# Optimization experiments

Hardware: AMD Instinct MI355X
Metric: run time of the kernel (lower is better)

Reference implementation:

```python
import jax, jax.numpy as jnp
import numpy as np

L, B, F, E, H, V, NL, K = 32, 128, 4096, 512, 512, 50000, 2, 20


def setup_inputs() -> dict:
    key = jax.random.key(0)
    ks = jax.random.split(key, 9)
    return {
        "dialog_encoder_inputs": jax.random.randint(ks[0], (L, B), 0, V),
        "fact_inputs": jax.random.normal(ks[1], (B, F, E), dtype=jnp.float32),
        "h": jax.random.normal(ks[2], (NL, B, H), dtype=jnp.float32),
        "c": jax.random.normal(ks[3], (NL, B, H), dtype=jnp.float32),
        "enc_emb": jax.random.normal(ks[4], (V, E), dtype=jnp.float32) * 0.02,
        "Aw": jax.random.normal(ks[5], (H, E), dtype=jnp.float32) * 0.04,
        "Ab": jnp.zeros((H,), dtype=jnp.float32),
        "Cw": jax.random.normal(ks[6], (H, E), dtype=jnp.float32) * 0.04,
        "Cb": jnp.zeros((H,), dtype=jnp.float32),
        "top_k": K,
    }


def reference(dialog_encoder_inputs, fact_inputs, h, c, enc_emb, Aw, Ab, Cw, Cb, top_k):
    # --- get_top_k_fact_average: embed dialog, score facts, gather top-k ---
    q = enc_emb[dialog_encoder_inputs].mean(axis=0)                # [B, E] mean-pooled query
    scores = jnp.einsum('be,bfe->bf', q, fact_inputs)              # [B, F] similarity
    _, idx = jax.lax.top_k(scores, top_k)                          # [B, K]
    topf = jnp.take_along_axis(fact_inputs, idx[:, :, None], axis=1)  # [B, K, E]

    # --- facts_forward: memory-network style hidden-state update ---
    fact_M = jnp.einsum('bke,he->bkh', topf, Aw) + Ab              # fact_linearA
    fact_C = jnp.einsum('bke,he->bkh', topf, Cw) + Cb              # fact_linearC

    def update(u):  # u: [NL, B, H]
        P = jax.nn.softmax(jnp.einsum('bke,lbe->lbk', topf, u), axis=-1)  # attn over facts
        o = jnp.einsum('lbk,bke->lbe', P, topf)                           # weighted fact avg
        return o + u

    return update(h), update(c), fact_M, fact_C
```

## Files before the change

kernel.cpp:

```cpp
#include <hip/hip_runtime.h>
#include <float.h>
#include <math.h>

#define LL 32
#define BB 128
#define FF 4096
#define EE 512
#define HH 512
#define NLAYER 2
#define KK 20

typedef float f4 __attribute__((ext_vector_type(4)));
typedef short bf16x8 __attribute__((ext_vector_type(8)));
typedef float f32x4 __attribute__((ext_vector_type(4)));

__device__ inline unsigned short bf16rne(float x) {
    unsigned u = __float_as_uint(x);
    u += 0x7fff + ((u >> 16) & 1);
    return (unsigned short)(u >> 16);
}

__global__ __launch_bounds__(256) void prep_kernel(const int* __restrict__ tok,
                                                   const float* __restrict__ emb,
                                                   float* __restrict__ q,
                                                   const float* __restrict__ Aw,
                                                   const float* __restrict__ Cw,
                                                   unsigned short* __restrict__ Wbf) {
    int bid = blockIdx.x;
    if (bid < 256) {
        int b = bid >> 1, eh = bid & 1;
        __shared__ int ts[LL];
        if (threadIdx.x < LL) ts[threadIdx.x] = tok[threadIdx.x * BB + b];
        __syncthreads();
        int e = eh * 256 + threadIdx.x;
        float acc = 0.f;
        #pragma unroll
        for (int l = 0; l < LL; ++l) acc += emb[(long)ts[l] * EE + e];
        q[b * EE + e] = acc * (1.0f / LL);
    } else {
        int cid = bid - 256;
        int matY = cid >> 8;
        int blkX = cid & 255;
        const float* W = matY ? Cw : Aw;
        unsigned short* dst = Wbf + (size_t)matY * HH * EE;
        int i = (blkX * 256 + threadIdx.x) * 4;
        float4 v = *(const float4*)(W + i);
        ushort4 o;
        o.x = bf16rne(v.x); o.y = bf16rne(v.y); o.z = bf16rne(v.z); o.w = bf16rne(v.w);
        *(ushort4*)(dst + i) = o;
    }
}

__global__ __launch_bounds__(256) void scores_kernel(const float* __restrict__ q,
                                                     const float* __restrict__ fact,
                                                     float* __restrict__ scores) {
    int b = blockIdx.y;
    int wave = threadIdx.x >> 6;
    int lane = threadIdx.x & 63;
    const f4* qv = (const f4*)(q + b * EE);
    f4 qa = qv[lane];
    f4 qb = qv[64 + lane];
    int f0 = (blockIdx.x * 4 + wave) * 8;
    float d[8];
    #pragma unroll
    for (int i = 0; i < 8; ++i) {
        const f4* fv = (const f4*)(fact + ((long)b * FF + f0 + i) * EE);
        f4 fa = __builtin_nontemporal_load(fv + lane);
        f4 fb = __builtin_nontemporal_load(fv + 64 + lane);
        f4 p = qa * fa + qb * fb;
        d[i] = p.x + p.y + p.z + p.w;
    }
    bool h32 = lane & 32;
    float e0, e1, e2, e3;
    {
        float s0 = __shfl_xor(d[0], 32), s1 = __shfl_xor(d[1], 32);
        float s2 = __shfl_xor(d[2], 32), s3 = __shfl_xor(d[3], 32);
        float s4 = __shfl_xor(d[4], 32), s5 = __shfl_xor(d[5], 32);
        float s6 = __shfl_xor(d[6], 32), s7 = __shfl_xor(d[7], 32);
        e0 = h32 ? d[4] + s4 : d[0] + s0;
        e1 = h32 ? d[5] + s5 : d[1] + s1;
        e2 = h32 ? d[6] + s6 : d[2] + s2;
        e3 = h32 ? d[7] + s7 : d[3] + s3;
    }
    bool h16 = lane & 16;
    float g0, g1;
    {
        float s0 = __shfl_xor(e0, 16), s1 = __shfl_xor(e1, 16);
        float s2 = __shfl_xor(e2, 16), s3 = __shfl_xor(e3, 16);
        g0 = h16 ? e2 + s2 : e0 + s0;
        g1 = h16 ? e3 + s3 : e1 + s1;
    }
    bool h8 = lane & 8;
    float hs;
    {
        float s0 = __shfl_xor(g0, 8), s1 = __shfl_xor(g1, 8);
        hs = h8 ? g1 + s1 : g0 + s0;
    }
    hs += __shfl_xor(hs, 4);
    hs += __shfl_xor(hs, 2);
    hs += __shfl_xor(hs, 1);
    if ((lane & 7) == 0) scores[b * FF + f0 + ((lane >> 3) & 7)] = hs;
}

__global__ __launch_bounds__(256) void fused_kernel(const float* __restrict__ scores,
                                                    const float* __restrict__ fact,
                                                    const float* __restrict__ hin,
                                                    const float* __restrict__ cin,
                                                    const unsigned short* __restrict__ Wbf,
                                                    const float* __restrict__ Ab,
                                                    const float* __restrict__ Cb,
                                                    float* __restrict__ out) {
    int b = blockIdx.x;
    __shared__ float vals[FF];
    __shared__ float tf[KK][EE];
    __shared__ unsigned short tfb[32 * EE];
    __shared__ unsigned long long wbest[4];
    __shared__ int sel[KK];
    int t = threadIdx.x;
    int wave = t >> 6, lane = t & 63;

    const float4* sv = (const float4*)(scores + b * FF);
    float4* vv = (float4*)vals;
    for (int i = t; i < FF / 4; i += 256) vv[i] = sv[i];
    {
        float4 z = {0, 0, 0, 0};
        for (int i = t; i < 12 * 1024 / 16; i += 256)
            *(float4*)((char*)tfb + 20 * 1024 + i * 16) = z;
    }
    __syncthreads();

    for (int it = 0; it < KK; ++it) {
        unsigned long long best = 0;
        #pragma unroll
        for (int s = 0; s < FF / 256; ++s) {
            int j = t + s * 256;
            unsigned u = __float_as_uint(vals[j]);
            u ^= ((int)u >> 31) | 0x80000000u;
            unsigned long long key = ((unsigned long long)u << 32) | (unsigned)(FF - 1 - j);
            if (key > best) best = key;
        }
        #pragma unroll
        for (int off = 32; off > 0; off >>= 1) {
            unsigned hi = (unsigned)(best >> 32), lo = (unsigned)best;
            unsigned ohi = __shfl_xor(hi, off, 64);
            unsigned olo = __shfl_xor(lo, off, 64);
            unsigned long long o = ((unsigned long long)ohi << 32) | olo;
            if (o > best) best = o;
        }
        if (lane == 0) wbest[wave] = best;
        __syncthreads();
        if (t == 0) {
            unsigned long long bb = wbest[0];
            if (wbest[1] > bb) bb = wbest[1];
            if (wbest[2] > bb) bb = wbest[2];
            if (wbest[3] > bb) bb = wbest[3];
            int idx = FF - 1 - (int)(bb & 0xFFFFFFFFu);
            sel[it] = idx;
            vals[idx] = -FLT_MAX;
        }
        __syncthreads();
    }

    for (int kk = 0; kk < KK; kk += 2) {
        int k = kk + (t >> 7);
        int e = t & 127;
        int src = sel[k];
        float4 v = *(const float4*)(fact + (((long)b * FF + src) * EE) + e * 4);
        *(float4*)&tf[k][e * 4] = v;
        ushort4 o;
        o.x = bf16rne(v.x); o.y = bf16rne(v.y); o.z = bf16rne(v.z); o.w = bf16rne(v.w);
        int byte = (k * 1024 + e * 8) ^ ((k & 7) << 4);
        *(ushort4*)((char*)tfb + byte) = o;
    }
    __syncthreads();

    {
        const float* u = (wave < 2 ? hin : cin) + ((size_t)(wave & 1) * BB + b) * EE;
        const float4* uv = (const float4*)u;
        float4 ua = uv[lane], ub = uv[64 + lane];
        float sk[KK];
        #pragma unroll
        for (int k = 0; k < KK; ++k) {
            const float4* tv = (const float4*)&tf[k][0];
            float4 ta = tv[lane], tb = tv[64 + lane];
            float d = ua.x * ta.x + ua.y * ta.y + ua.z * ta.z + ua.w * ta.w
                    + ub.x * tb.x + ub.y * tb.y + ub.z * tb.z + ub.w * tb.w;
            #pragma unroll
            for (int off = 32; off > 0; off >>= 1) d += __shfl_xor(d, off, 64);
            sk[k] = d;
        }
        float m = sk[0];
        #pragma unroll
        for (int k = 1; k < KK; ++k) m = fmaxf(m, sk[k]);
        float sum = 0.f;
        #pragma unroll
        for (int k = 0; k < KK; ++k) { sk[k] = __expf(sk[k] - m); sum += sk[k]; }
        float inv = 1.f / sum;
        float4 oa = {0, 0, 0, 0}, ob = {0, 0, 0, 0};
        #pragma unroll
        for (int k = 0; k < KK; ++k) {
            float p = sk[k] * inv;
            const float4* tv = (const float4*)&tf[k][0];
            float4 ta = tv[lane], tb = tv[64 + lane];
            oa.x += p * ta.x; oa.y += p * ta.y; oa.z += p * ta.z; oa.w += p * ta.w;
            ob.x += p * tb.x; ob.y += p * tb.y; ob.z += p * tb.z; ob.w += p * tb.w;
        }
        oa.x += ua.x; oa.y += ua.y; oa.z += ua.z; oa.w += ua.w;
        ob.x += ub.x; ob.y += ub.y; ob.z += ub.z; ob.w += ub.w;
        float* obase = out + (size_t)(wave < 2 ? 0 : NLAYER * BB * HH)
                           + ((size_t)(wave & 1) * BB + b) * HH;
        float4* ov = (float4*)obase;
        ov[lane] = oa;
        ov[64 + lane] = ob;
    }

    {
        int lrow = lane & 15, lk = lane >> 4;
        for (int mat = 0; mat < 2; ++mat) {
            const unsigned short* W = Wbf + (size_t)mat * HH * EE;
            const float* bias = mat ? Cb : Ab;
            float* O = out + (size_t)2 * NLAYER * BB * HH
                           + (size_t)mat * BB * KK * HH + (size_t)b * KK * HH;
            f32x4 acc[2][8];
            #pragma unroll
            for (int m = 0; m < 2; ++m)
                #pragma unroll
                for (int n = 0; n < 8; ++n) acc[m][n] = (f32x4){0, 0, 0, 0};
            const unsigned short* wbase = W + (size_t)(wave * 128 + lrow) * EE + lk * 8;
            #pragma unroll 2
            for (int ks = 0; ks < 16; ++ks) {
                int col2 = (ks * 32 + lk * 8) * 2;
                int byte0 = (lrow * 1024 + col2) ^ ((lrow & 7) << 4);
                bf16x8 a0 = *(const bf16x8*)((const char*)tfb + byte0);
                int r1 = 16 + lrow;
                int byte1 = (r1 * 1024 + col2) ^ ((r1 & 7) << 4);
                bf16x8 a1 = *(const bf16x8*)((const char*)tfb + byte1);
                #pragma unroll
                for (int n = 0; n < 8; ++n) {
                    bf16x8 bfrag = *(const bf16x8*)(wbase + (size_t)n * 16 * EE + ks * 32);
                    acc[0][n] = __builtin_amdgcn_mfma_f32_16x16x32_bf16(a0, bfrag, acc[0][n], 0, 0, 0);
                    acc[1][n] = __builtin_amdgcn_mfma_f32_16x16x32_bf16(a1, bfrag, acc[1][n], 0, 0, 0);
                }
            }
            #pragma unroll
            for (int n = 0; n < 8; ++n) {
                int h = wave * 128 + n * 16 + lrow;
                float bv = bias[h];
                #pragma unroll
                for (int r = 0; r < 4; ++r) {
                    int k0 = lk * 4 + r;
                    O[(size_t)k0 * HH + h] = acc[0][n][r] + bv;
                    int k1 = 16 + lk * 4 + r;
                    if (k1 < KK) O[(size_t)k1 * HH + h] = acc[1][n][r] + bv;
                }
            }
        }
    }
}

extern "C" void kernel_launch(void* const* d_in, const int* in_sizes, int n_in,
                              void* d_out, int out_size, void* d_ws, size_t ws_size,
                              hipStream_t stream) {
    const int* tok = (const int*)d_in[0];
    const float* fact = (const float*)d_in[1];
    const float* hin = (const float*)d_in[2];
    const float* cin = (const float*)d_in[3];
    const float* emb = (const float*)d_in[4];
    const float* Aw = (const float*)d_in[5];
    const float* Ab = (const float*)d_in[6];
    const float* Cw = (const float*)d_in[7];
    const float* Cb = (const float*)d_in[8];
    float* out = (float*)d_out;

    float* ws = (float*)d_ws;
    float* q = ws;
    float* scores = ws + 65536;
    unsigned short* Wbf = (unsigned short*)(ws + 65536 + 524288);

    prep_kernel<<<768, 256, 0, stream>>>(tok, emb, q, Aw, Cw, Wbf);
    scores_kernel<<<dim3(FF / 32, BB), 256, 0, stream>>>(q, fact, scores);
    fused_kernel<<<BB, 256, 0, stream>>>(scores, fact, hin, cin, Wbf, Ab, Cb, out);
}
```

Baseline: 238.5 us.

## Split fused kernel into top-k/update and fact projection kernels, register-resident top-k

The single per-batch fused kernel is split in two. The first does top-k selection and the h/c update, and writes the selected facts as bf16 to workspace. The second runs the fact_M/fact_C MFMA projection on a (B, 2) grid, so twice as many blocks cover the GPU's compute units. Top-k selection now keeps the 16 score keys per thread in registers and invalidates the winner by key match, instead of rescanning LDS each iteration. The cost is one extra kernel launch and a global round trip for the bf16 top-k facts.

New measurement: 220.5 us. -7.6%, faster.

```diff
diff --git a/kernel.cpp b/kernel.cpp
--- a/kernel.cpp
+++ b/kernel.cpp
@@ -102,49 +102,44 @@
     if ((lane & 7) == 0) scores[b * FF + f0 + ((lane >> 3) & 7)] = hs;
 }
 
-__global__ __launch_bounds__(256) void fused_kernel(const float* __restrict__ scores,
-                                                    const float* __restrict__ fact,
-                                                    const float* __restrict__ hin,
-                                                    const float* __restrict__ cin,
-                                                    const unsigned short* __restrict__ Wbf,
-                                                    const float* __restrict__ Ab,
-                                                    const float* __restrict__ Cb,
-                                                    float* __restrict__ out) {
+__global__ __launch_bounds__(256) void topk_update_kernel(const float* __restrict__ scores,
+                                                          const float* __restrict__ fact,
+                                                          const float* __restrict__ hin,
+                                                          const float* __restrict__ cin,
+                                                          unsigned short* __restrict__ topfb,
+                                                          float* __restrict__ out) {
     int b = blockIdx.x;
-    __shared__ float vals[FF];
     __shared__ float tf[KK][EE];
-    __shared__ unsigned short tfb[32 * EE];
     __shared__ unsigned long long wbest[4];
+    __shared__ unsigned long long wkey_s;
     __shared__ int sel[KK];
     int t = threadIdx.x;
     int wave = t >> 6, lane = t & 63;
 
-    const float4* sv = (const float4*)(scores + b * FF);
-    float4* vv = (float4*)vals;
-    for (int i = t; i < FF / 4; i += 256) vv[i] = sv[i];
-    {
-        float4 z = {0, 0, 0, 0};
-        for (int i = t; i < 12 * 1024 / 16; i += 256)
-            *(float4*)((char*)tfb + 20 * 1024 + i * 16) = z;
-    }
-    __syncthreads();
+    unsigned long long keys[16];
+    {
+        const float4* sv = (const float4*)(scores + b * FF);
+        #pragma unroll
+        for (int s = 0; s < 4; ++s) {
+            float4 v = sv[t + 256 * s];
+            float vc[4] = {v.x, v.y, v.z, v.w};
+            #pragma unroll
+            for (int c = 0; c < 4; ++c) {
+                int idx = 4 * (t + 256 * s) + c;
+                unsigned u = __float_as_uint(vc[c]);
+                u ^= ((int)u >> 31) | 0x80000000u;
+                keys[s * 4 + c] = ((unsigned long long)u << 32) | (unsigned)(FF - 1 - idx);
+            }
+        }
+    }
 
     for (int it = 0; it < KK; ++it) {
-        unsigned long long best = 0;
-        #pragma unroll
-        for (int s = 0; s < FF / 256; ++s) {
-            int j = t + s * 256;
-            unsigned u = __float_as_uint(vals[j]);
-            u ^= ((int)u >> 31) | 0x80000000u;
-            unsigned long long key = ((unsigned long long)u << 32) | (unsigned)(FF - 1 - j);
-            if (key > best) best = key;
-        }
+        unsigned long long best = keys[0];
+        #pragma unroll
+        for (int i = 1; i < 16; ++i) best = keys[i] > best ? keys[i] : best;
         #pragma unroll
         for (int off = 32; off > 0; off >>= 1) {
-            unsigned hi = (unsigned)(best >> 32), lo = (unsigned)best;
-            unsigned ohi = __shfl_xor(hi, off, 64);
-            unsigned olo = __shfl_xor(lo, off, 64);
-            unsigned long long o = ((unsigned long long)ohi << 32) | olo;
+            unsigned long long o = __shfl_xor(best, off, 64);
             if (o > best) best = o;
         }
         if (lane == 0) wbest[wave] = best;
@@ -154,11 +149,14 @@
             if (wbest[1] > bb) bb = wbest[1];
             if (wbest[2] > bb) bb = wbest[2];
             if (wbest[3] > bb) bb = wbest[3];
-            int idx = FF - 1 - (int)(bb & 0xFFFFFFFFu);
-            sel[it] = idx;
-            vals[idx] = -FLT_MAX;
+            wkey_s = bb;
+            sel[it] = FF - 1 - (int)(bb & 0xFFFFFFFFu);
         }
         __syncthreads();
+        unsigned long long wk = wkey_s;
+        #pragma unroll
+        for (int i = 0; i < 16; ++i)
+            if (keys[i] == wk) keys[i] = 0;
     }
 
     for (int kk = 0; kk < KK; kk += 2) {
@@ -169,91 +167,109 @@
         *(float4*)&tf[k][e * 4] = v;
         ushort4 o;
         o.x = bf16rne(v.x); o.y = bf16rne(v.y); o.z = bf16rne(v.z); o.w = bf16rne(v.w);
-        int byte = (k * 1024 + e * 8) ^ ((k & 7) << 4);
-        *(ushort4*)((char*)tfb + byte) = o;
+        *(ushort4*)(topfb + ((size_t)b * KK + k) * EE + e * 4) = o;
     }
     __syncthreads();
 
-    {
-        const float* u = (wave < 2 ? hin : cin) + ((size_t)(wave & 1) * BB + b) * EE;
-        const float4* uv = (const float4*)u;
-        float4 ua = uv[lane], ub = uv[64 + lane];
-        float sk[KK];
-        #pragma unroll
-        for (int k = 0; k < KK; ++k) {
-            const float4* tv = (const float4*)&tf[k][0];
-            float4 ta = tv[lane], tb = tv[64 + lane];
-            float d = ua.x * ta.x + ua.y * ta.y + ua.z * ta.z + ua.w * ta.w
-                    + ub.x * tb.x + ub.y * tb.y + ub.z * tb.z + ub.w * tb.w;
-            #pragma unroll
-            for (int off = 32; off > 0; off >>= 1) d += __shfl_xor(d, off, 64);
-            sk[k] = d;
-        }
-        float m = sk[0];
-        #pragma unroll
-        for (int k = 1; k < KK; ++k) m = fmaxf(m, sk[k]);
-        float sum = 0.f;
-        #pragma unroll
-        for (int k = 0; k < KK; ++k) { sk[k] = __expf(sk[k] - m); sum += sk[k]; }
-        float inv = 1.f / sum;
-        float4 oa = {0, 0, 0, 0}, ob = {0, 0, 0, 0};
-        #pragma unroll
-        for (int k = 0; k < KK; ++k) {
-            float p = sk[k] * inv;
-            const float4* tv = (const float4*)&tf[k][0];
-            float4 ta = tv[lane], tb = tv[64 + lane];
-            oa.x += p * ta.x; oa.y += p * ta.y; oa.z += p * ta.z; oa.w += p * ta.w;
-            ob.x += p * tb.x; ob.y += p * tb.y; ob.z += p * tb.z; ob.w += p * tb.w;
-        }
-        oa.x += ua.x; oa.y += ua.y; oa.z += ua.z; oa.w += ua.w;
-        ob.x += ub.x; ob.y += ub.y; ob.z += ub.z; ob.w += ub.w;
-        float* obase = out + (size_t)(wave < 2 ? 0 : NLAYER * BB * HH)
-                           + ((size_t)(wave & 1) * BB + b) * HH;
-        float4* ov = (float4*)obase;
-        ov[lane] = oa;
-        ov[64 + lane] = ob;
-    }
-
-    {
-        int lrow = lane & 15, lk = lane >> 4;
-        for (int mat = 0; mat < 2; ++mat) {
-            const unsigned short* W = Wbf + (size_t)mat * HH * EE;
-            const float* bias = mat ? Cb : Ab;
-            float* O = out + (size_t)2 * NLAYER * BB * HH
-                           + (size_t)mat * BB * KK * HH + (size_t)b * KK * HH;
-            f32x4 acc[2][8];
-            #pragma unroll
-            for (int m = 0; m < 2; ++m)
-                #pragma unroll
-                for (int n = 0; n < 8; ++n) acc[m][n] = (f32x4){0, 0, 0, 0};
-            const unsigned short* wbase = W + (size_t)(wave * 128 + lrow) * EE + lk * 8;
-            #pragma unroll 2
-            for (int ks = 0; ks < 16; ++ks) {
-                int col2 = (ks * 32 + lk * 8) * 2;
-                int byte0 = (lrow * 1024 + col2) ^ ((lrow & 7) << 4);
-                bf16x8 a0 = *(const bf16x8*)((const char*)tfb + byte0);
-                int r1 = 16 + lrow;
-                int byte1 = (r1 * 1024 + col2) ^ ((r1 & 7) << 4);
-                bf16x8 a1 = *(const bf16x8*)((const char*)tfb + byte1);
-                #pragma unroll
-                for (int n = 0; n < 8; ++n) {
-                    bf16x8 bfrag = *(const bf16x8*)(wbase + (size_t)n * 16 * EE + ks * 32);
-                    acc[0][n] = __builtin_amdgcn_mfma_f32_16x16x32_bf16(a0, bfrag, acc[0][n], 0, 0, 0);
-                    acc[1][n] = __builtin_amdgcn_mfma_f32_16x16x32_bf16(a1, bfrag, acc[1][n], 0, 0, 0);
-                }
-            }
-            #pragma unroll
-            for (int n = 0; n < 8; ++n) {
-                int h = wave * 128 + n * 16 + lrow;
-                float bv = bias[h];
-                #pragma unroll
-                for (int r = 0; r < 4; ++r) {
-                    int k0 = lk * 4 + r;
-                    O[(size_t)k0 * HH + h] = acc[0][n][r] + bv;
-                    int k1 = 16 + lk * 4 + r;
-                    if (k1 < KK) O[(size_t)k1 * HH + h] = acc[1][n][r] + bv;
-                }
-            }
+    const float* u = (wave < 2 ? hin : cin) + ((size_t)(wave & 1) * BB + b) * EE;
+    const float4* uv = (const float4*)u;
+    float4 ua = uv[lane], ub = uv[64 + lane];
+    float sk[KK];
+    #pragma unroll
+    for (int k = 0; k < KK; ++k) {
+        const float4* tv = (const float4*)&tf[k][0];
+        float4 ta = tv[lane], tb = tv[64 + lane];
+        float d = ua.x * ta.x + ua.y * ta.y + ua.z * ta.z + ua.w * ta.w
+                + ub.x * tb.x + ub.y * tb.y + ub.z * tb.z + ub.w * tb.w;
+        #pragma unroll
+        for (int off = 32; off > 0; off >>= 1) d += __shfl_xor(d, off, 64);
+        sk[k] = d;
+    }
+    float m = sk[0];
+    #pragma unroll
+    for (int k = 1; k < KK; ++k) m = fmaxf(m, sk[k]);
+    float sum = 0.f;
+    #pragma unroll
+    for (int k = 0; k < KK; ++k) { sk[k] = __expf(sk[k] - m); sum += sk[k]; }
+    float inv = 1.f / sum;
+    float4 oa = {0, 0, 0, 0}, ob = {0, 0, 0, 0};
+    #pragma unroll
+    for (int k = 0; k < KK; ++k) {
+        float p = sk[k] * inv;
+        const float4* tv = (const float4*)&tf[k][0];
+        float4 ta = tv[lane], tb = tv[64 + lane];
+        oa.x += p * ta.x; oa.y += p * ta.y; oa.z += p * ta.z; oa.w += p * ta.w;
+        ob.x += p * tb.x; ob.y += p * tb.y; ob.z += p * tb.z; ob.w += p * tb.w;
+    }
+    oa.x += ua.x; oa.y += ua.y; oa.z += ua.z; oa.w += ua.w;
+    ob.x += ub.x; ob.y += ub.y; ob.z += ub.z; ob.w += ub.w;
+    float* obase = out + (size_t)(wave < 2 ? 0 : NLAYER * BB * HH)
+                       + ((size_t)(wave & 1) * BB + b) * HH;
+    float4* ov = (float4*)obase;
+    ov[lane] = oa;
+    ov[64 + lane] = ob;
+}
+
+__global__ __launch_bounds__(256) void factmc_kernel(const unsigned short* __restrict__ topfb,
+                                                     const unsigned short* __restrict__ Wbf,
+                                                     const float* __restrict__ Ab,
+                                                     const float* __restrict__ Cb,
+                                                     float* __restrict__ out) {
+    int b = blockIdx.x, mat = blockIdx.y;
+    const unsigned short* W = Wbf + (size_t)mat * HH * EE;
+    const float* bias = mat ? Cb : Ab;
+    float* O = out + (size_t)2 * NLAYER * BB * HH
+                   + (size_t)mat * BB * KK * HH + (size_t)b * KK * HH;
+
+    __shared__ unsigned short tf[32 * EE];
+    {
+        const unsigned short* src = topfb + (size_t)b * KK * EE;
+        for (int ib = threadIdx.x; ib < KK * EE / 8; ib += 256) {
+            int row = ib >> 6;
+            int cb = ib & 63;
+            float4 v = *(const float4*)(src + row * EE + cb * 8);
+            int byte = (row * 1024 + cb * 16) ^ ((row & 7) << 4);
+            *(float4*)((char*)tf + byte) = v;
+        }
+    }
+    __syncthreads();
+
+    int wave = threadIdx.x >> 6, lane = threadIdx.x & 63;
+    int lrow = lane & 15, lk = lane >> 4;
+    f32x4 acc[2][8];
+    #pragma unroll
+    for (int m = 0; m < 2; ++m)
+        #pragma unroll
+        for (int n = 0; n < 8; ++n) acc[m][n] = (f32x4){0, 0, 0, 0};
+
+    const unsigned short* wbase = W + (size_t)(wave * 128 + lrow) * EE + lk * 8;
+
+    #pragma unroll 2
+    for (int ks = 0; ks < 16; ++ks) {
+        int col2 = (ks * 32 + lk * 8) * 2;
+        int byte0 = (lrow * 1024 + col2) ^ ((lrow & 7) << 4);
+        bf16x8 a0 = *(const bf16x8*)((const char*)tf + byte0);
+        int r1 = 16 + lrow;
+        int byte1 = (r1 * 1024 + col2) ^ ((r1 & 7) << 4);
+        bf16x8 a1 = *(const bf16x8*)((const char*)tf + byte1);
+        #pragma unroll
+        for (int n = 0; n < 8; ++n) {
+            bf16x8 bfrag = *(const bf16x8*)(wbase + (size_t)n * 16 * EE + ks * 32);
+            acc[0][n] = __builtin_amdgcn_mfma_f32_16x16x32_bf16(a0, bfrag, acc[0][n], 0, 0, 0);
+            acc[1][n] = __builtin_amdgcn_mfma_f32_16x16x32_bf16(a1, bfrag, acc[1][n], 0, 0, 0);
+        }
+    }
+
+    #pragma unroll
+    for (int n = 0; n < 8; ++n) {
+        int h = wave * 128 + n * 16 + lrow;
+        float bv = bias[h];
+        #pragma unroll
+        for (int r = 0; r < 4; ++r) {
+            int k0 = lk * 4 + r;
+            O[(size_t)k0 * HH + h] = acc[0][n][r] + bv;
+            int k1 = 16 + lk * 4 + r;
+            if (k1 < KK) O[(size_t)k1 * HH + h] = acc[1][n][r] + bv;
         }
     }
 }
@@ -275,9 +291,11 @@
     float* ws = (float*)d_ws;
     float* q = ws;
     float* scores = ws + 65536;
-    unsigned short* Wbf = (unsigned short*)(ws + 65536 + 524288);
+    unsigned short* topfb = (unsigned short*)(ws + 65536 + 524288);
+    unsigned short* Wbf = (unsigned short*)(ws + 65536 + 524288 + 655360);
 
     prep_kernel<<<768, 256, 0, stream>>>(tok, emb, q, Aw, Cw, Wbf);
     scores_kernel<<<dim3(FF / 32, BB), 256, 0, stream>>>(q, fact, scores);
-    fused_kernel<<<BB, 256, 0, stream>>>(scores, fact, hin, cin, Wbf, Ab, Cb, out);
-}
+    topk_update_kernel<<<BB, 256, 0, stream>>>(scores, fact, hin, cin, topfb, out);
+    factmc_kernel<<<dim3(BB, 2), 256, 0, stream>>>(topfb, Wbf, Ab, Cb, out);
+}
```
